# Optimization experiments

Measured on AMD Instinct MI355X. Metric: run time of the kernel, lower is better.

The kernel has to match this reference:

```python
import jax, jax.numpy as jnp
import numpy as np


def setup_inputs() -> dict:
    key = jax.random.key(0)
    k1, k2, k3, k4 = jax.random.split(key, 4)
    n_smps, n_fcns, d_in, d_out = 16384, 2048, 32, 32
    GAIN = 1e-5  # xavier gain used by init_wts / init_offsets
    x = jax.random.normal(k1, (n_smps, d_in), dtype=jnp.float32)
    ctrs = jax.random.normal(k2, (n_fcns, d_in), dtype=jnp.float32)
    wts = jax.random.normal(k3, (n_fcns, d_in, d_out), dtype=jnp.float32) * GAIN
    offsets = jax.random.normal(k4, (n_fcns, d_out), dtype=jnp.float32) * GAIN
    return {"x": x, "ctrs": ctrs, "wts": wts, "offsets": offsets, "k": 4}


def reference(x, ctrs, wts, offsets, k):
    # --- knn_do equivalent (done under no_grad in torch) ---
    # squared Euclidean distance: (n_smps, n_fcns)
    x_sg = jax.lax.stop_gradient(x)
    c_sg = jax.lax.stop_gradient(ctrs)
    d2 = (jnp.sum(x_sg * x_sg, axis=1, keepdims=True)
          - 2.0 * (x_sg @ c_sg.T)
          + jnp.sum(c_sg * c_sg, axis=1)[None, :])
    _, idx = jax.lax.top_k(-d2, k)  # (n_smps, k), nearest centers

    # --- gather per-neighbor local linear models ---
    sel_wts = wts[idx]        # (n_smps, k, d_in, d_out)
    sel_ctrs = ctrs[idx]      # (n_smps, k, d_in)
    sel_offs = offsets[idx]   # (n_smps, k, d_out)

    applied_wts = jnp.sum(sel_wts, axis=1)  # (n_smps, d_in, d_out)
    # offsets minus sum over neighbors/d_in of wts * ctrs
    applied_offsets = (jnp.sum(sel_offs, axis=1)
                       - jnp.einsum('nkde,nkd->ne', sel_wts, sel_ctrs))
    # y = x @ applied_wts + applied_offsets, per sample
    y = jnp.einsum('nde,nd->ne', applied_wts, x) + applied_offsets
    return y
```

## Files before the change

### kernel.cpp

```cpp
#include <hip/hip_runtime.h>
#include <math.h>

typedef short bf16x8 __attribute__((ext_vector_type(8)));
typedef float f32x4  __attribute__((ext_vector_type(4)));

#define N_SMPS 16384
#define N_FCNS 2048
#define D_IN 32
#define D_OUT 32
#define KNN 4
#define SPLITS 4
#define CPS 512
#define TILES 32
#define POOL 48
#define SMP 16

__device__ __forceinline__ unsigned umin_u(unsigned a, unsigned b) { return a < b ? a : b; }
__device__ __forceinline__ unsigned umax_u(unsigned a, unsigned b) { return a > b ? a : b; }

__device__ __forceinline__ unsigned short bf16_rne(float f) {
  unsigned b = __float_as_uint(f);
  unsigned r = b + 0x7FFFu + ((b >> 16) & 1u);
  return (unsigned short)(r >> 16);
}

#define OFF_XH   0u
#define OFF_CH   1048576u
#define OFF_HB   (OFF_CH + 131072u)
#define OFF_WB   (OFF_HB + 8192u)

#define NX4 (N_SMPS * D_IN / 4)
#define NC4 (N_FCNS * D_IN / 4)
#define NW4 (N_FCNS * D_IN * D_OUT / 4)
#define NTOT (NX4 + NC4 + NW4)

__global__ __launch_bounds__(256) void k_prep(
    const float* __restrict__ x, const float* __restrict__ ctrs,
    const float* __restrict__ wts,
    unsigned short* __restrict__ xh, unsigned short* __restrict__ ch,
    unsigned short* __restrict__ wb, float* __restrict__ hb)
{
  const int gt = blockIdx.x * 256 + threadIdx.x;
  const float* src; unsigned short* dst; int i4;
  if (gt < NX4)            { src = x;    dst = xh; i4 = gt; }
  else if (gt < NX4 + NC4) { src = ctrs; dst = ch; i4 = gt - NX4; }
  else                     { src = wts;  dst = wb; i4 = gt - (NX4 + NC4); }
  float4 v = ((const float4*)src)[i4];
  ushort4 o;
  o.x = bf16_rne(v.x); o.y = bf16_rne(v.y);
  o.z = bf16_rne(v.z); o.w = bf16_rne(v.w);
  ((ushort4*)dst)[i4] = o;

  if (gt < N_FCNS) {
    const float4* cp4 = (const float4*)(ctrs + (size_t)gt * D_IN);
    float a = 0.f;
    #pragma unroll
    for (int q = 0; q < 8; ++q) {
      float4 c = cp4[q];
      a += c.x * c.x + c.y * c.y + c.z * c.z + c.w * c.w;
    }
    hb[gt] = -0.5f * a;
  }
}

__global__ __launch_bounds__(256) void k_mega(
    const unsigned short* __restrict__ xh, const unsigned short* __restrict__ ch,
    const float* __restrict__ hb,
    const float* __restrict__ x, const float* __restrict__ ctrs,
    const unsigned short* __restrict__ wb, const float* __restrict__ offs,
    float* __restrict__ y)
{
  __shared__ __align__(16) char u_mem[16640];
  __shared__ float    s_hb[SPLITS * CPS];
  __shared__ unsigned s_pool[SMP][POOL];
  __shared__ double   s_pd2[SMP][POOL];
  __shared__ int      s_pix[SMP][POOL];
  __shared__ int      s_sel[SMP][KNN];

  unsigned* s_cand = (unsigned*)u_mem;
  float*    s_diff = (float*)u_mem;
  float4*   s_part = (float4*)(u_mem + 8448);

  const int tid = threadIdx.x;
  const int lane = tid & 63;
  const int w = __builtin_amdgcn_readfirstlane(tid >> 6);
  const int col = lane & 15;
  const int quad = lane >> 4;
  const int sbase = blockIdx.x * SMP;
  const int nbase0 = w * CPS;

  #pragma unroll
  for (int r = 0; r < CPS / 64; ++r)
    s_hb[nbase0 + r * 64 + lane] = hb[nbase0 + r * 64 + lane];

  const bf16x8 ah =
      *(const bf16x8*)(xh + (size_t)(sbase + col) * D_IN + quad * 8);

  unsigned ls[4][4];
  #pragma unroll
  for (int r = 0; r < 4; ++r)
    #pragma unroll
    for (int e = 0; e < 4; ++e) ls[r][e] = 0u;

  const unsigned short* chb =
      ch + (size_t)nbase0 * D_IN + (size_t)col * D_IN + quad * 8;
  #define BLOAD(t) (*(const bf16x8*)(chb + (size_t)(t) * 16 * D_IN))
  #define HLOAD(t) (s_hb[nbase0 + (t) * 16 + col])

  __syncthreads();

  bf16x8 bh[4];
  float  hv[4];
  #pragma unroll
  for (int p = 0; p < 4; ++p) { bh[p] = BLOAD(p); hv[p] = HLOAD(p); }

  for (int t = 0; t < TILES; t += 4) {
    #pragma unroll
    for (int p = 0; p < 4; ++p) {
      {
        f32x4 acc = {0.f, 0.f, 0.f, 0.f};
        acc = __builtin_amdgcn_mfma_f32_16x16x32_bf16(ah, bh[p], acc, 0, 0, 0);
        const unsigned tc = (unsigned)((t + p) * 16 + col);
        const float hvv = hv[p];
        #pragma unroll
        for (int r = 0; r < 4; ++r) {
          const float uu = acc[r] + hvv;
          unsigned b = __float_as_uint(uu);
          unsigned m = b ^ ((unsigned)((int)b >> 31) | 0x80000000u);
          unsigned key = (m & 0xFFFFFE00u) | tc;
          unsigned t0 = umin_u(ls[r][0], key); ls[r][0] = umax_u(ls[r][0], key);
          unsigned t1 = umin_u(ls[r][1], t0);  ls[r][1] = umax_u(ls[r][1], t0);
          unsigned t2 = umin_u(ls[r][2], t1);  ls[r][2] = umax_u(ls[r][2], t1);
          ls[r][3] = umax_u(ls[r][3], t2);
        }
      }
      const int tn = (t + 4 + p) & (TILES - 1);
      bh[p] = BLOAD(tn);
      hv[p] = HLOAD(tn);
    }
  }
  #undef BLOAD
  #undef HLOAD

  #pragma unroll
  for (int r = 0; r < 4; ++r) {
    const int row = quad * 4 + r;
    *(uint4*)&s_cand[(((w * 16) + row) * 16 + col) * 4] =
        make_uint4(ls[r][0], ls[r][1], ls[r][2], ls[r][3]);
  }
  __syncthreads();

  if (tid < 128) {
    const int sl = tid >> 3;
    const int g  = tid & 7;
    const int wv = g >> 1;
    const int chh = (g & 1) * 8;
    unsigned q0 = 0, q1 = 0, q2 = 0, q3 = 0, q4 = 0, q5 = 0;
    #pragma unroll
    for (int c2 = 0; c2 < 8; ++c2) {
      uint4 kv = *(const uint4*)&s_cand[(((wv * 16) + sl) * 16 + chh + c2) * 4];
      unsigned ks[4] = {kv.x, kv.y, kv.z, kv.w};
      #pragma unroll
      for (int e = 0; e < 4; ++e) {
        unsigned key = ks[e];
        unsigned t0 = umin_u(q0, key); q0 = umax_u(q0, key);
        unsigned t1 = umin_u(q1, t0);  q1 = umax_u(q1, t0);
        unsigned t2 = umin_u(q2, t1);  q2 = umax_u(q2, t1);
        unsigned t3 = umin_u(q3, t2);  q3 = umax_u(q3, t2);
        unsigned t4 = umin_u(q4, t3);  q4 = umax_u(q4, t3);
        q5 = umax_u(q5, t4);
      }
    }
    unsigned* op = &s_pool[sl][g * 6];
    op[0] = q0; op[1] = q1; op[2] = q2;
    op[3] = q3; op[4] = q4; op[5] = q5;
  }
  __syncthreads();

  for (int c = tid; c < SMP * POOL; c += 256) {
    const int sl = c / POOL;
    const int p = c - sl * POOL;
    const unsigned key = s_pool[sl][p];
    const int wv = p / 12;
    const int j = wv * CPS + (int)(key & 0x1FFu);
    const float4* xp4 = (const float4*)(x + (size_t)(sbase + sl) * D_IN);
    const float4* cp4 = (const float4*)(ctrs + (size_t)j * D_IN);
    double d2a = 0.0, d2b = 0.0;
    #pragma unroll
    for (int q = 0; q < 8; ++q) {
      float4 cv = cp4[q];
      float4 xv = xp4[q];
      double df0 = (double)xv.x - (double)cv.x;
      double df1 = (double)xv.y - (double)cv.y;
      double df2 = (double)xv.z - (double)cv.z;
      double df3 = (double)xv.w - (double)cv.w;
      d2a = fma(df0, df0, d2a);
      d2b = fma(df1, df1, d2b);
      d2a = fma(df2, df2, d2a);
      d2b = fma(df3, df3, d2b);
    }
    s_pd2[sl][p] = d2a + d2b;
    s_pix[sl][p] = j;
  }
  __syncthreads();

  if (tid < SMP) {
    double bd[4]; int b4[4];
    #pragma unroll
    for (int e = 0; e < 4; ++e) { bd[e] = 1e300; b4[e] = 0x7fffffff; }
    for (int m = 0; m < POOL; ++m) {
      const double d2 = s_pd2[tid][m];
      const int j = s_pix[tid][m];
      bool ins = (d2 < bd[3]) || (d2 == bd[3] && j < b4[3]);
      if (ins) {
        bd[3] = d2; b4[3] = j;
        #pragma unroll
        for (int q = 3; q > 0; --q) {
          bool sw = (bd[q] < bd[q - 1]) ||
                    (bd[q] == bd[q - 1] && b4[q] < b4[q - 1]);
          if (sw) {
            double td = bd[q]; bd[q] = bd[q - 1]; bd[q - 1] = td;
            int    tj = b4[q]; b4[q] = b4[q - 1]; b4[q - 1] = tj;
          }
        }
      }
    }
    #pragma unroll
    for (int q = 0; q < 4; ++q) s_sel[tid][q] = b4[q];
  }
  __syncthreads();

  #pragma unroll
  for (int r = 0; r < SMP * KNN * D_IN / 256; ++r) {
    int v = r * 256 + tid;
    int d = v & 31; int p = v >> 5;
    int sl = p >> 2; int j = p & 3;
    int f = s_sel[sl][j];
    s_diff[(sl * KNN + j) * (D_IN + 1) + d] =
        x[(size_t)(sbase + sl) * D_IN + d] - ctrs[(size_t)f * D_IN + d];
  }
  __syncthreads();

  #pragma unroll
  for (int r = 0; r < 2; ++r) {
    const int slot = r * 256 + tid;
    const int sl = slot >> 5;
    const int j  = (slot >> 3) & 3;
    const int eq = slot & 7;
    const int f = s_sel[sl][j];
    const uint2* wp = (const uint2*)(wb + (size_t)f * (D_IN * D_OUT));
    float4 acc = ((const float4*)(offs + (size_t)f * D_OUT))[eq];
    #pragma unroll
    for (int d = 0; d < D_IN; ++d) {
      uint2 wv = wp[d * 8 + eq];
      float w0 = __uint_as_float(wv.x << 16);
      float w1 = __uint_as_float(wv.x & 0xFFFF0000u);
      float w2 = __uint_as_float(wv.y << 16);
      float w3 = __uint_as_float(wv.y & 0xFFFF0000u);
      float xc = s_diff[(sl * KNN + j) * (D_IN + 1) + d];
      acc.x = fmaf(xc, w0, acc.x);
      acc.y = fmaf(xc, w1, acc.y);
      acc.z = fmaf(xc, w2, acc.z);
      acc.w = fmaf(xc, w3, acc.w);
    }
    s_part[(sl * KNN + j) * 8 + eq] = acc;
  }
  __syncthreads();

  #pragma unroll
  for (int r = 0; r < 2; ++r) {
    const int slot = r * 256 + tid;
    const int sl = slot >> 5;
    const int j  = (slot >> 3) & 3;
    const int eq = slot & 7;
    if (j == 0) {
      float4 a = s_part[(sl * KNN + 0) * 8 + eq];
      float4 b = s_part[(sl * KNN + 1) * 8 + eq];
      float4 c = s_part[(sl * KNN + 2) * 8 + eq];
      float4 e = s_part[(sl * KNN + 3) * 8 + eq];
      float4 o;
      o.x = (a.x + b.x) + (c.x + e.x);
      o.y = (a.y + b.y) + (c.y + e.y);
      o.z = (a.z + b.z) + (c.z + e.z);
      o.w = (a.w + b.w) + (c.w + e.w);
      ((float4*)(y + (size_t)(sbase + sl) * D_OUT))[eq] = o;
    }
  }
}

extern "C" void kernel_launch(void* const* d_in, const int* in_sizes, int n_in,
                              void* d_out, int out_size, void* d_ws, size_t ws_size,
                              hipStream_t stream) {
  const float* x    = (const float*)d_in[0];
  const float* ctrs = (const float*)d_in[1];
  const float* wts  = (const float*)d_in[2];
  const float* offs = (const float*)d_in[3];
  float* y = (float*)d_out;

  char* ws = (char*)d_ws;
  unsigned short* xh = (unsigned short*)(ws + OFF_XH);
  unsigned short* ch = (unsigned short*)(ws + OFF_CH);
  float*          hb = (float*)(ws + OFF_HB);
  unsigned short* wb = (unsigned short*)(ws + OFF_WB);

  k_prep<<<NTOT / 256, 256, 0, stream>>>(x, ctrs, wts, xh, ch, wb, hb);
  k_mega<<<N_SMPS / SMP, 256, 0, stream>>>(xh, ch, hb, x, ctrs, wb, offs, y);
}
```

Measured before the change: 111.1 us.

## Split center scan across eight waves with two-phase candidate merge

Doubles the block to 512 threads so eight waves each scan 256 centers instead of four waves scanning 512, which halves each wave's serial MFMA/top-4 loop. The candidate merge runs in two phases reusing the same shared buffer, with an XOR swizzle to reduce LDS bank conflicts. The double-precision pool arrays are aliased into the union buffer to cut LDS footprint, and the key index field shrinks to 8 bits. It adds extra barriers and a serialized merge done by only 64 threads, and it changes occupancy.

```diff
diff --git a/kernel.cpp b/kernel.cpp
--- a/kernel.cpp
+++ b/kernel.cpp
@@ -9,11 +9,12 @@
 #define D_IN 32
 #define D_OUT 32
 #define KNN 4
-#define SPLITS 4
-#define CPS 512
-#define TILES 32
+#define WAVES 8
+#define CPS 256
+#define TILES 16
 #define POOL 48
 #define SMP 16
+#define BLK 512
 
 __device__ __forceinline__ unsigned umin_u(unsigned a, unsigned b) { return a < b ? a : b; }
 __device__ __forceinline__ unsigned umax_u(unsigned a, unsigned b) { return a > b ? a : b; }
@@ -63,7 +64,7 @@
   }
 }
 
-__global__ __launch_bounds__(256) void k_mega(
+__global__ __launch_bounds__(BLK, 8) void k_mega(
     const unsigned short* __restrict__ xh, const unsigned short* __restrict__ ch,
     const float* __restrict__ hb,
     const float* __restrict__ x, const float* __restrict__ ctrs,
@@ -71,13 +72,13 @@
     float* __restrict__ y)
 {
   __shared__ __align__(16) char u_mem[16640];
-  __shared__ float    s_hb[SPLITS * CPS];
+  __shared__ float    s_hb[WAVES * CPS];
   __shared__ unsigned s_pool[SMP][POOL];
-  __shared__ double   s_pd2[SMP][POOL];
-  __shared__ int      s_pix[SMP][POOL];
   __shared__ int      s_sel[SMP][KNN];
 
   unsigned* s_cand = (unsigned*)u_mem;
+  double*   s_pd2  = (double*)u_mem;
+  int*      s_pix  = (int*)(u_mem + 6144);
   float*    s_diff = (float*)u_mem;
   float4*   s_part = (float4*)(u_mem + 8448);
 
@@ -127,7 +128,7 @@
           const float uu = acc[r] + hvv;
           unsigned b = __float_as_uint(uu);
           unsigned m = b ^ ((unsigned)((int)b >> 31) | 0x80000000u);
-          unsigned key = (m & 0xFFFFFE00u) | tc;
+          unsigned key = (m & 0xFFFFFF00u) | tc;
           unsigned t0 = umin_u(ls[r][0], key); ls[r][0] = umax_u(ls[r][0], key);
           unsigned t1 = umin_u(ls[r][1], t0);  ls[r][1] = umax_u(ls[r][1], t0);
           unsigned t2 = umin_u(ls[r][2], t1);  ls[r][2] = umax_u(ls[r][2], t1);
@@ -142,23 +143,23 @@
   #undef BLOAD
   #undef HLOAD
 
-  #pragma unroll
-  for (int r = 0; r < 4; ++r) {
-    const int row = quad * 4 + r;
-    *(uint4*)&s_cand[(((w * 16) + row) * 16 + col) * 4] =
-        make_uint4(ls[r][0], ls[r][1], ls[r][2], ls[r][3]);
-  }
-  __syncthreads();
-
-  if (tid < 128) {
-    const int sl = tid >> 3;
-    const int g  = tid & 7;
-    const int wv = g >> 1;
-    const int chh = (g & 1) * 8;
+  if (w < 4) {
+    #pragma unroll
+    for (int r = 0; r < 4; ++r) {
+      const int row = quad * 4 + r;
+      *(uint4*)&s_cand[(((w * 16) + row) * 16 + (col ^ row)) * 4] =
+          make_uint4(ls[r][0], ls[r][1], ls[r][2], ls[r][3]);
+    }
+  }
+  __syncthreads();
+  if (tid < 64) {
+    const int sl = tid >> 2;
+    const int slot = tid & 3;
+    const int g = slot;
     unsigned q0 = 0, q1 = 0, q2 = 0, q3 = 0, q4 = 0, q5 = 0;
     #pragma unroll
-    for (int c2 = 0; c2 < 8; ++c2) {
-      uint4 kv = *(const uint4*)&s_cand[(((wv * 16) + sl) * 16 + chh + c2) * 4];
+    for (int c2 = 0; c2 < 16; ++c2) {
+      uint4 kv = *(const uint4*)&s_cand[(((slot * 16) + sl) * 16 + (c2 ^ sl)) * 4];
       unsigned ks[4] = {kv.x, kv.y, kv.z, kv.w};
       #pragma unroll
       for (int e = 0; e < 4; ++e) {
@@ -176,13 +177,47 @@
     op[3] = q3; op[4] = q4; op[5] = q5;
   }
   __syncthreads();
-
-  for (int c = tid; c < SMP * POOL; c += 256) {
+  if (w >= 4) {
+    #pragma unroll
+    for (int r = 0; r < 4; ++r) {
+      const int row = quad * 4 + r;
+      *(uint4*)&s_cand[((((w - 4) * 16) + row) * 16 + (col ^ row)) * 4] =
+          make_uint4(ls[r][0], ls[r][1], ls[r][2], ls[r][3]);
+    }
+  }
+  __syncthreads();
+  if (tid < 64) {
+    const int sl = tid >> 2;
+    const int slot = tid & 3;
+    const int g = 4 + slot;
+    unsigned q0 = 0, q1 = 0, q2 = 0, q3 = 0, q4 = 0, q5 = 0;
+    #pragma unroll
+    for (int c2 = 0; c2 < 16; ++c2) {
+      uint4 kv = *(const uint4*)&s_cand[(((slot * 16) + sl) * 16 + (c2 ^ sl)) * 4];
+      unsigned ks[4] = {kv.x, kv.y, kv.z, kv.w};
+      #pragma unroll
+      for (int e = 0; e < 4; ++e) {
+        unsigned key = ks[e];
+        unsigned t0 = umin_u(q0, key); q0 = umax_u(q0, key);
+        unsigned t1 = umin_u(q1, t0);  q1 = umax_u(q1, t0);
+        unsigned t2 = umin_u(q2, t1);  q2 = umax_u(q2, t1);
+        unsigned t3 = umin_u(q3, t2);  q3 = umax_u(q3, t2);
+        unsigned t4 = umin_u(q4, t3);  q4 = umax_u(q4, t3);
+        q5 = umax_u(q5, t4);
+      }
+    }
+    unsigned* op = &s_pool[sl][g * 6];
+    op[0] = q0; op[1] = q1; op[2] = q2;
+    op[3] = q3; op[4] = q4; op[5] = q5;
+  }
+  __syncthreads();
+
+  for (int c = tid; c < SMP * POOL; c += BLK) {
     const int sl = c / POOL;
     const int p = c - sl * POOL;
     const unsigned key = s_pool[sl][p];
-    const int wv = p / 12;
-    const int j = wv * CPS + (int)(key & 0x1FFu);
+    const int wv = p / 6;
+    const int j = wv * CPS + (int)(key & 0xFFu);
     const float4* xp4 = (const float4*)(x + (size_t)(sbase + sl) * D_IN);
     const float4* cp4 = (const float4*)(ctrs + (size_t)j * D_IN);
     double d2a = 0.0, d2b = 0.0;
@@ -199,8 +234,8 @@
       d2a = fma(df2, df2, d2a);
       d2b = fma(df3, df3, d2b);
     }
-    s_pd2[sl][p] = d2a + d2b;
-    s_pix[sl][p] = j;
+    s_pd2[sl * POOL + p] = d2a + d2b;
+    s_pix[sl * POOL + p] = j;
   }
   __syncthreads();
 
@@ -209,8 +244,8 @@
     #pragma unroll
     for (int e = 0; e < 4; ++e) { bd[e] = 1e300; b4[e] = 0x7fffffff; }
     for (int m = 0; m < POOL; ++m) {
-      const double d2 = s_pd2[tid][m];
-      const int j = s_pix[tid][m];
+      const double d2 = s_pd2[tid * POOL + m];
+      const int j = s_pix[tid * POOL + m];
       bool ins = (d2 < bd[3]) || (d2 == bd[3] && j < b4[3]);
       if (ins) {
         bd[3] = d2; b4[3] = j;
@@ -231,8 +266,8 @@
   __syncthreads();
 
   #pragma unroll
-  for (int r = 0; r < SMP * KNN * D_IN / 256; ++r) {
-    int v = r * 256 + tid;
+  for (int r = 0; r < SMP * KNN * D_IN / BLK; ++r) {
+    int v = r * BLK + tid;
     int d = v & 31; int p = v >> 5;
     int sl = p >> 2; int j = p & 3;
     int f = s_sel[sl][j];
@@ -241,9 +276,8 @@
   }
   __syncthreads();
 
-  #pragma unroll
-  for (int r = 0; r < 2; ++r) {
-    const int slot = r * 256 + tid;
+  {
+    const int slot = tid;
     const int sl = slot >> 5;
     const int j  = (slot >> 3) & 3;
     const int eq = slot & 7;
@@ -267,9 +301,8 @@
   }
   __syncthreads();
 
-  #pragma unroll
-  for (int r = 0; r < 2; ++r) {
-    const int slot = r * 256 + tid;
+  {
+    const int slot = tid;
     const int sl = slot >> 5;
     const int j  = (slot >> 3) & 3;
     const int eq = slot & 7;
@@ -304,5 +337,5 @@
   unsigned short* wb = (unsigned short*)(ws + OFF_WB);
 
   k_prep<<<NTOT / 256, 256, 0, stream>>>(x, ctrs, wts, xh, ch, wb, hb);
-  k_mega<<<N_SMPS / SMP, 256, 0, stream>>>(xh, ch, hb, x, ctrs, wb, offs, y);
+  k_mega<<<N_SMPS / SMP, BLK, 0, stream>>>(xh, ch, hb, x, ctrs, wb, offs, y);
 }
```

Measured after the change: 115.5 us. 4.0% more time.

## Drop bf16 prepass for x and wts; convert x in-kernel, read fp32 weights

Applied to the files above, without the earlier changes.

The prep kernel now converts only the centers to bf16 and computes their half-norms. It no longer converts all of x (2 MB) and wts (8 MB) to bf16 in a separate pass. The main kernel converts its 16 sample rows to bf16 in shared memory and reads fp32 weights directly in the gather/apply stage. This removes about 10 MB of read plus 5 MB of write in the prep pass, at the cost of doubling the bytes of weights gathered per selected neighbor. It also gains accuracy, since weights are no longer rounded to bf16.

```diff
diff --git a/kernel.cpp b/kernel.cpp
--- a/kernel.cpp
+++ b/kernel.cpp
@@ -24,32 +24,21 @@
   return (unsigned short)(r >> 16);
 }
 
-#define OFF_XH   0u
-#define OFF_CH   1048576u
-#define OFF_HB   (OFF_CH + 131072u)
-#define OFF_WB   (OFF_HB + 8192u)
-
-#define NX4 (N_SMPS * D_IN / 4)
+#define OFF_CH   0u
+#define OFF_HB   131072u
+
 #define NC4 (N_FCNS * D_IN / 4)
-#define NW4 (N_FCNS * D_IN * D_OUT / 4)
-#define NTOT (NX4 + NC4 + NW4)
 
 __global__ __launch_bounds__(256) void k_prep(
-    const float* __restrict__ x, const float* __restrict__ ctrs,
-    const float* __restrict__ wts,
-    unsigned short* __restrict__ xh, unsigned short* __restrict__ ch,
-    unsigned short* __restrict__ wb, float* __restrict__ hb)
+    const float* __restrict__ ctrs,
+    unsigned short* __restrict__ ch, float* __restrict__ hb)
 {
   const int gt = blockIdx.x * 256 + threadIdx.x;
-  const float* src; unsigned short* dst; int i4;
-  if (gt < NX4)            { src = x;    dst = xh; i4 = gt; }
-  else if (gt < NX4 + NC4) { src = ctrs; dst = ch; i4 = gt - NX4; }
-  else                     { src = wts;  dst = wb; i4 = gt - (NX4 + NC4); }
-  float4 v = ((const float4*)src)[i4];
+  float4 v = ((const float4*)ctrs)[gt];
   ushort4 o;
   o.x = bf16_rne(v.x); o.y = bf16_rne(v.y);
   o.z = bf16_rne(v.z); o.w = bf16_rne(v.w);
-  ((ushort4*)dst)[i4] = o;
+  ((ushort4*)ch)[gt] = o;
 
   if (gt < N_FCNS) {
     const float4* cp4 = (const float4*)(ctrs + (size_t)gt * D_IN);
@@ -64,10 +53,10 @@
 }
 
 __global__ __launch_bounds__(256) void k_mega(
-    const unsigned short* __restrict__ xh, const unsigned short* __restrict__ ch,
+    const unsigned short* __restrict__ ch,
     const float* __restrict__ hb,
     const float* __restrict__ x, const float* __restrict__ ctrs,
-    const unsigned short* __restrict__ wb, const float* __restrict__ offs,
+    const float* __restrict__ wts, const float* __restrict__ offs,
     float* __restrict__ y)
 {
   __shared__ __align__(16) char u_mem[16640];
@@ -76,6 +65,7 @@
   __shared__ double   s_pd2[SMP][POOL];
   __shared__ int      s_pix[SMP][POOL];
   __shared__ int      s_sel[SMP][KNN];
+  __shared__ __align__(16) unsigned short s_xh[SMP * D_IN];
 
   unsigned* s_cand = (unsigned*)u_mem;
   float*    s_diff = (float*)u_mem;
@@ -93,8 +83,19 @@
   for (int r = 0; r < CPS / 64; ++r)
     s_hb[nbase0 + r * 64 + lane] = hb[nbase0 + r * 64 + lane];
 
-  const bf16x8 ah =
-      *(const bf16x8*)(xh + (size_t)(sbase + col) * D_IN + quad * 8);
+  if (tid < 128) {
+    const int s = tid >> 3;
+    const int q = tid & 7;
+    float4 v = ((const float4*)(x + (size_t)(sbase + s) * D_IN))[q];
+    ushort4 o;
+    o.x = bf16_rne(v.x); o.y = bf16_rne(v.y);
+    o.z = bf16_rne(v.z); o.w = bf16_rne(v.w);
+    ((ushort4*)s_xh)[tid] = o;
+  }
+
+  __syncthreads();
+
+  const bf16x8 ah = *(const bf16x8*)(s_xh + col * D_IN + quad * 8);
 
   unsigned ls[4][4];
   #pragma unroll
@@ -106,8 +107,6 @@
       ch + (size_t)nbase0 * D_IN + (size_t)col * D_IN + quad * 8;
   #define BLOAD(t) (*(const bf16x8*)(chb + (size_t)(t) * 16 * D_IN))
   #define HLOAD(t) (s_hb[nbase0 + (t) * 16 + col])
-
-  __syncthreads();
 
   bf16x8 bh[4];
   float  hv[4];
@@ -248,20 +247,16 @@
     const int j  = (slot >> 3) & 3;
     const int eq = slot & 7;
     const int f = s_sel[sl][j];
-    const uint2* wp = (const uint2*)(wb + (size_t)f * (D_IN * D_OUT));
+    const float4* wp = (const float4*)(wts + (size_t)f * (D_IN * D_OUT));
     float4 acc = ((const float4*)(offs + (size_t)f * D_OUT))[eq];
     #pragma unroll
     for (int d = 0; d < D_IN; ++d) {
-      uint2 wv = wp[d * 8 + eq];
-      float w0 = __uint_as_float(wv.x << 16);
-      float w1 = __uint_as_float(wv.x & 0xFFFF0000u);
-      float w2 = __uint_as_float(wv.y << 16);
-      float w3 = __uint_as_float(wv.y & 0xFFFF0000u);
+      float4 wv = wp[d * 8 + eq];
       float xc = s_diff[(sl * KNN + j) * (D_IN + 1) + d];
-      acc.x = fmaf(xc, w0, acc.x);
-      acc.y = fmaf(xc, w1, acc.y);
-      acc.z = fmaf(xc, w2, acc.z);
-      acc.w = fmaf(xc, w3, acc.w);
+      acc.x = fmaf(xc, wv.x, acc.x);
+      acc.y = fmaf(xc, wv.y, acc.y);
+      acc.z = fmaf(xc, wv.z, acc.z);
+      acc.w = fmaf(xc, wv.w, acc.w);
     }
     s_part[(sl * KNN + j) * 8 + eq] = acc;
   }
@@ -298,11 +293,9 @@
   float* y = (float*)d_out;
 
   char* ws = (char*)d_ws;
-  unsigned short* xh = (unsigned short*)(ws + OFF_XH);
   unsigned short* ch = (unsigned short*)(ws + OFF_CH);
   float*          hb = (float*)(ws + OFF_HB);
-  unsigned short* wb = (unsigned short*)(ws + OFF_WB);
-
-  k_prep<<<NTOT / 256, 256, 0, stream>>>(x, ctrs, wts, xh, ch, wb, hb);
-  k_mega<<<N_SMPS / SMP, 256, 0, stream>>>(xh, ch, hb, x, ctrs, wb, offs, y);
+
+  k_prep<<<NC4 / 256, 256, 0, stream>>>(ctrs, ch, hb);
+  k_mega<<<N_SMPS / SMP, 256, 0, stream>>>(ch, hb, x, ctrs, wts, offs, y);
 }
```

New measurement: 120.9 us. +8.8%, slower.
